# Kernel tuning notes

Hardware: AMD Instinct MI355X
Metric: run time of the kernel (lower is better)

Reference implementation:

```python
import jax, jax.numpy as jnp
import numpy as np

NUM_NOD = 6
MAX_PREV = 5
NUM_EDGE = 20  # (1+5)*5//2 + 5*(6-5)
D = 1024
H = 8
LN_EPS = 1e-6


def setup_inputs() -> dict:
    key = jax.random.key(0)
    ks = jax.random.split(key, 12)
    B, S = 8, 1024
    scale = 1.0 / np.sqrt(D)
    return {
        "inputs": jax.random.normal(ks[0], (B, S, D), jnp.float32),
        "ew": jax.random.uniform(ks[1], (NUM_NOD, 3), jnp.float32),
        "act_w": jax.random.uniform(ks[2], (NUM_NOD,), jnp.float32),
        "We": jax.random.normal(ks[3], (NUM_EDGE, D, D), jnp.float32) * scale,
        "be": jnp.zeros((NUM_EDGE, D), jnp.float32),
        "Wq": jax.random.normal(ks[4], (NUM_NOD, D, D), jnp.float32) * scale,
        "Wk": jax.random.normal(ks[5], (NUM_NOD, D, D), jnp.float32) * scale,
        "Wv": jax.random.normal(ks[6], (NUM_NOD, D, D), jnp.float32) * scale,
        "Wo": jax.random.normal(ks[7], (NUM_NOD, D, D), jnp.float32) * scale,
        "ln_g": jnp.ones((D,), jnp.float32),
        "ln_b": jnp.zeros((D,), jnp.float32),
    }


def _layernorm(x, g, b):
    mu = jnp.mean(x, axis=-1, keepdims=True)
    var = jnp.mean(jnp.square(x - mu), axis=-1, keepdims=True)
    return (x - mu) * jax.lax.rsqrt(var + LN_EPS) * g + b


def _mha(q, k, v, wq, wk, wv, wo):
    B, S, d = q.shape
    dh = d // H
    qh = (q @ wq).reshape(B, S, H, dh)
    kh = (k @ wk).reshape(B, S, H, dh)
    vh = (v @ wv).reshape(B, S, H, dh)
    scores = jnp.einsum("bqhd,bkhd->bhqk", qh, kh) / jnp.sqrt(jnp.asarray(dh, q.dtype))
    attn = jax.nn.softmax(scores, axis=-1)
    ctx = jnp.einsum("bhqk,bkhd->bqhd", attn, vh).reshape(B, S, d)
    return ctx @ wo


def reference(inputs, ew, act_w, We, be, Wq, Wk, Wv, Wo, ln_g, ln_b):
    # Fixed (deterministic) routing: node act = attention (q,k,v) for all nodes.
    # Edge op = linear (sel_ope 3). q from node c-1, k from earliest visible node,
    # v from the middle of the visible window; gated by Gumbel weights ew/act_w.
    nodes = {-1: inputs}
    lind = 0
    for c in range(NUM_NOD):
        nsrc = min(c + 1, MAX_PREV)
        snode = c - nsrc
        eq, ek, ev = lind + nsrc - 1, lind, lind + nsrc // 2
        in_q, in_k, in_v = c - 1, snode, snode + nsrc // 2
        q = ew[c, 0] * (nodes[in_q] @ We[eq] + be[eq])
        k = ew[c, 1] * (nodes[in_k] @ We[ek] + be[ek])
        v = ew[c, 2] * (nodes[in_v] @ We[ev] + be[ev])
        o = _mha(q, k, v, Wq[c], Wk[c], Wv[c], Wo[c])
        nodes[c] = act_w[c] * o + q  # gated attention + residual
        lind += nsrc
    # only node 5 is unconsumed under this routing
    out = nodes[NUM_NOD - 1]
    return _layernorm(out, ln_g, ln_b)
```

## Files before the change

### kernel.cpp

```cpp
#include <hip/hip_runtime.h>
#include <stdint.h>

#define DD 1024
#define MM 8192

typedef unsigned short u16;
typedef __attribute__((ext_vector_type(8))) short s16x8;
typedef __attribute__((ext_vector_type(4))) short s16x4;
typedef __attribute__((ext_vector_type(8))) __bf16 bf16x8;
typedef __attribute__((ext_vector_type(4))) float f32x4;

__device__ inline u16 f2bf(float f) {
  uint32_t u = __builtin_bit_cast(uint32_t, f);
  u += 0x7fffu + ((u >> 16) & 1u);
  return (u16)(u >> 16);
}
__device__ inline u16 f2bf_rn(float f) {
  return __builtin_bit_cast(u16, (__bf16)f);
}
__device__ inline float bf2f(u16 h) {
  return __builtin_bit_cast(float, (uint32_t)h << 16);
}
__device__ inline f32x4 mfma32(s16x8 a, s16x8 b, f32x4 c) {
  return __builtin_amdgcn_mfma_f32_16x16x32_bf16(
      __builtin_bit_cast(bf16x8, a), __builtin_bit_cast(bf16x8, b), c, 0, 0, 0);
}

__global__ __launch_bounds__(256) void k_cvt(const float* __restrict__ in,
                                             u16* __restrict__ out, int n8) {
  int i = blockIdx.x * 256 + threadIdx.x;
  if (i >= n8) return;
  const float4* p = (const float4*)in;
  float4 a = p[2 * i], b = p[2 * i + 1];
  union { s16x8 v; u16 u[8]; } r;
  r.u[0] = f2bf(a.x); r.u[1] = f2bf(a.y); r.u[2] = f2bf(a.z); r.u[3] = f2bf(a.w);
  r.u[4] = f2bf(b.x); r.u[5] = f2bf(b.y); r.u[6] = f2bf(b.z); r.u[7] = f2bf(b.w);
  ((s16x8*)out)[i] = r.v;
}

struct WSrcs { const float* p[7]; };
__global__ __launch_bounds__(256) void k_wtransN(WSrcs ws, u16* __restrict__ pool) {
  __shared__ u16 t[32][33];
  int m = blockIdx.z;
  const float* src = ws.p[m];
  u16* dst = pool + (size_t)m * DD * DD;
  int c0 = blockIdx.x * 32, r0 = blockIdx.y * 32;
  int tx = threadIdx.x, ty = threadIdx.y;
  #pragma unroll
  for (int j = 0; j < 4; ++j)
    t[ty + j * 8][tx] = f2bf(src[(size_t)(r0 + ty + j * 8) * DD + c0 + tx]);
  __syncthreads();
  #pragma unroll
  for (int j = 0; j < 4; ++j)
    dst[(size_t)(c0 + ty + j * 8) * DD + r0 + tx] = t[tx][ty + j * 8];
}

__global__ __launch_bounds__(256) void k_vtrans(const u16* __restrict__ vp,
                                                u16* __restrict__ vt) {
  __shared__ u16 t[32][33];
  int bh = blockIdx.z, b = bh >> 3, h = bh & 7;
  int s0 = blockIdx.x * 32, d0 = blockIdx.y * 32;
  int tx = threadIdx.x, ty = threadIdx.y;
  #pragma unroll
  for (int j = 0; j < 4; ++j)
    t[ty + j * 8][tx] = vp[(size_t)(b * 1024 + s0 + ty + j * 8) * DD + h * 128 + d0 + tx];
  __syncthreads();
  #pragma unroll
  for (int j = 0; j < 4; ++j)
    vt[((size_t)bh * 128 + d0 + ty + j * 8) * 1024 + s0 + tx] = t[tx][ty + j * 8];
}

struct GemmJob {
  const u16* A; const u16* Bt; const float* bias; const u16* resid;
  float* f32out;
  u16* out0; const float* s0p; float s0c;
  u16* out1; const float* s1p;
  u16* out2; const float* s2p;
};
struct GemmBatch { GemmJob j[3]; };

__global__ __launch_bounds__(256, 2) void k_gemmN(GemmBatch gb) {
  const GemmJob jb = gb.j[blockIdx.z];
  __shared__ u16 As[128 * 64];
  __shared__ u16 Bs[128 * 64];
  const int tid = threadIdx.x;
  const int lane = tid & 63, wave = tid >> 6;
  const int g = lane >> 4, r15 = lane & 15;
  const int m0 = blockIdx.x * 128, n0 = blockIdx.y * 128;
  const int wm = (wave >> 1) * 64, wn = (wave & 1) * 64;
  f32x4 acc[4][4] = {};
  for (int kt = 0; kt < 16; ++kt) {
    const int k0 = kt * 64;
    __syncthreads();
    #pragma unroll
    for (int i = 0; i < 4; ++i) {
      int c = tid + i * 256;
      int row = c >> 3, kc = (c & 7) ^ (row & 7);
      __builtin_amdgcn_global_load_lds(
          (__attribute__((address_space(1))) void*)(jb.A + (size_t)(m0 + row) * DD + k0 + kc * 8),
          (__attribute__((address_space(3))) void*)(As + c * 8), 16, 0, 0);
    }
    #pragma unroll
    for (int i = 0; i < 4; ++i) {
      int c = tid + i * 256;
      int row = c >> 3, kc = (c & 7) ^ (row & 7);
      __builtin_amdgcn_global_load_lds(
          (__attribute__((address_space(1))) void*)(jb.Bt + (size_t)(n0 + row) * DD + k0 + kc * 8),
          (__attribute__((address_space(3))) void*)(Bs + c * 8), 16, 0, 0);
    }
    __syncthreads();
    #pragma unroll
    for (int ks = 0; ks < 2; ++ks) {
      s16x8 af[4], bfr[4];
      #pragma unroll
      for (int f = 0; f < 4; ++f) {
        int row = wm + f * 16 + r15;
        int kc = (ks * 4 + g) ^ (row & 7);
        af[f] = *(const s16x8*)(As + row * 64 + kc * 8);
        int rowb = wn + f * 16 + r15;
        int kcb = (ks * 4 + g) ^ (rowb & 7);
        bfr[f] = *(const s16x8*)(Bs + rowb * 64 + kcb * 8);
      }
      #pragma unroll
      for (int fm = 0; fm < 4; ++fm)
        #pragma unroll
        for (int fn = 0; fn < 4; ++fn)
          acc[fm][fn] = mfma32(af[fm], bfr[fn], acc[fm][fn]);
    }
  }
  const float s0 = jb.s0c * (jb.s0p ? jb.s0p[0] : 1.0f);
  const float s1 = (jb.s1p ? jb.s1p[0] : 1.0f);
  const float s2 = (jb.s2p ? jb.s2p[0] : 1.0f);
  #pragma unroll
  for (int fm = 0; fm < 4; ++fm) {
    #pragma unroll
    for (int fn = 0; fn < 4; ++fn) {
      int col = n0 + wn + fn * 16 + r15;
      float bcol = jb.bias ? jb.bias[col] : 0.0f;
      #pragma unroll
      for (int j = 0; j < 4; ++j) {
        int row = m0 + wm + fm * 16 + g * 4 + j;
        size_t idx = (size_t)row * DD + col;
        float v = acc[fm][fn][j] + bcol;
        float v0 = s0 * v + (jb.resid ? bf2f(jb.resid[idx]) : 0.0f);
        if (jb.out0) jb.out0[idx] = f2bf(v0);
        if (jb.f32out) jb.f32out[idx] = v0;
        if (jb.out1) jb.out1[idx] = f2bf(s1 * v);
        if (jb.out2) jb.out2[idx] = f2bf(s2 * v);
      }
    }
  }
}

__global__ __launch_bounds__(256, 2) void k_attn(
    const u16* __restrict__ qp, const u16* __restrict__ kp,
    const u16* __restrict__ vt, u16* __restrict__ ctx) {
  __shared__ u16 Ks[2][64 * 128];
  __shared__ u16 Vs[2][128 * 72];
  const int lin = blockIdx.y * gridDim.x + blockIdx.x;
  const int m = lin >> 3;
  const int bh = (lin & 7) * 8 + (m & 7);
  const int q0 = (m >> 3) * 128;
  const int b = bh >> 3, h = bh & 7;
  const int tid = threadIdx.x, lane = tid & 63, wave = tid >> 6;
  const int g = lane >> 4, r15 = lane & 15;
  s16x8 qf[2][4];
  #pragma unroll
  for (int qg = 0; qg < 2; ++qg) {
    const u16* qb = qp + (size_t)(b * 1024 + q0 + wave * 32 + qg * 16 + r15) * DD + h * 128;
    #pragma unroll
    for (int kk = 0; kk < 4; ++kk) qf[qg][kk] = *(const s16x8*)(qb + kk * 32 + g * 8);
  }
  f32x4 o0[8] = {}, o1[8] = {};
  float mrow0 = -1e30f, lrow0 = 0.0f, mrow1 = -1e30f, lrow1 = 0.0f;
  const u16* kpb = kp + (size_t)b * 1024 * DD + h * 128;
  const u16* vtb = vt + (size_t)bh * 128 * 1024;

  s16x8 vreg[4];
  auto stageK = [&](int t, int buf) {
    #pragma unroll
    for (int i = 0; i < 4; ++i) {
      int c = tid + i * 256;
      int row = c >> 4, kc = (c & 15) ^ (row & 7);
      __builtin_amdgcn_global_load_lds(
          (__attribute__((address_space(1))) void*)(kpb + (size_t)(t * 64 + row) * DD + kc * 8),
          (__attribute__((address_space(3))) void*)(Ks[buf] + c * 8), 16, 0, 0);
    }
  };
  auto loadV = [&](int t) {
    #pragma unroll
    for (int i = 0; i < 4; ++i) {
      int c = tid + i * 256;
      int row = c >> 3, kc = c & 7;
      vreg[i] = *(const s16x8*)(vtb + (size_t)row * 1024 + t * 64 + kc * 8);
    }
  };
  auto writeV = [&](int buf) {
    #pragma unroll
    for (int i = 0; i < 4; ++i) {
      int c = tid + i * 256;
      int row = c >> 3, kc = c & 7;
      *(s16x8*)(Vs[buf] + row * 72 + kc * 8) = vreg[i];
    }
  };

  stageK(0, 0);
  loadV(0);
  writeV(0);
  __syncthreads();

  union pk_t { s16x8 v; u16 u[8]; };
  for (int t = 0; t < 16; ++t) {
    const int cur = t & 1;
    if (t < 15) {
      stageK(t + 1, cur ^ 1);
      loadV(t + 1);
    }
    f32x4 s0[4] = {}, s1[4] = {};
    __builtin_amdgcn_s_setprio(1);
    #pragma unroll
    for (int sub = 0; sub < 4; ++sub) {
      const int krow = sub * 16 + r15;
      #pragma unroll
      for (int kk = 0; kk < 4; ++kk) {
        int slot = (kk * 4 + g) ^ (krow & 7);
        s16x8 kf = *(const s16x8*)(Ks[cur] + krow * 128 + slot * 8);
        s0[sub] = mfma32(kf, qf[0][kk], s0[sub]);
        s1[sub] = mfma32(kf, qf[1][kk], s1[sub]);
      }
    }
    __builtin_amdgcn_s_setprio(0);
    pk_t pa0[2], pa1[2];
    {
      float tm = -1e30f;
      #pragma unroll
      for (int sub = 0; sub < 4; ++sub)
        tm = fmaxf(fmaxf(fmaxf(s0[sub][0], s0[sub][1]), fmaxf(s0[sub][2], s0[sub][3])), tm);
      tm = fmaxf(tm, __shfl_xor(tm, 16));
      tm = fmaxf(tm, __shfl_xor(tm, 32));
      if (!__all(tm - mrow0 <= 8.0f)) {
        float mnew = fmaxf(mrow0, tm);
        float corr = exp2f(mrow0 - mnew);
        lrow0 *= corr;
        #pragma unroll
        for (int j = 0; j < 4; ++j) {
          float cj = __shfl(corr, (lane & 48) + g * 4 + j);
          #pragma unroll
          for (int dt = 0; dt < 8; ++dt) o0[dt][j] *= cj;
        }
        mrow0 = mnew;
      }
      float ps = 0.0f;
      #pragma unroll
      for (int sub = 0; sub < 4; ++sub)
        #pragma unroll
        for (int j = 0; j < 4; ++j) {
          float pe = exp2f(s0[sub][j] - mrow0);
          ps += pe;
          pa0[sub >> 1].u[(sub & 1) * 4 + j] = f2bf_rn(pe);
        }
      ps += __shfl_xor(ps, 16);
      ps += __shfl_xor(ps, 32);
      lrow0 += ps;
    }
    {
      float tm = -1e30f;
      #pragma unroll
      for (int sub = 0; sub < 4; ++sub)
        tm = fmaxf(fmaxf(fmaxf(s1[sub][0], s1[sub][1]), fmaxf(s1[sub][2], s1[sub][3])), tm);
      tm = fmaxf(tm, __shfl_xor(tm, 16));
      tm = fmaxf(tm, __shfl_xor(tm, 32));
      if (!__all(tm - mrow1 <= 8.0f)) {
        float mnew = fmaxf(mrow1, tm);
        float corr = exp2f(mrow1 - mnew);
        lrow1 *= corr;
        #pragma unroll
        for (int j = 0; j < 4; ++j) {
          float cj = __shfl(corr, (lane & 48) + g * 4 + j);
          #pragma unroll
          for (int dt = 0; dt < 8; ++dt) o1[dt][j] *= cj;
        }
        mrow1 = mnew;
      }
      float ps = 0.0f;
      #pragma unroll
      for (int sub = 0; sub < 4; ++sub)
        #pragma unroll
        for (int j = 0; j < 4; ++j) {
          float pe = exp2f(s1[sub][j] - mrow1);
          ps += pe;
          pa1[sub >> 1].u[(sub & 1) * 4 + j] = f2bf_rn(pe);
        }
      ps += __shfl_xor(ps, 16);
      ps += __shfl_xor(ps, 32);
      lrow1 += ps;
    }
    if (t < 15) writeV(cur ^ 1);
    __builtin_amdgcn_s_setprio(1);
    #pragma unroll
    for (int p01 = 0; p01 < 2; ++p01) {
      #pragma unroll
      for (int dt = 0; dt < 8; ++dt) {
        union { s16x8 v; s16x4 h[2]; } vv;
        const u16* vbase = Vs[cur] + (dt * 16 + r15) * 72 + p01 * 32 + g * 4;
        vv.h[0] = *(const s16x4*)(vbase);
        vv.h[1] = *(const s16x4*)(vbase + 16);
        o0[dt] = mfma32(pa0[p01].v, vv.v, o0[dt]);
        o1[dt] = mfma32(pa1[p01].v, vv.v, o1[dt]);
      }
    }
    __builtin_amdgcn_s_setprio(0);
    __syncthreads();
  }
  {
    float inv = 1.0f / lrow0;
    #pragma unroll
    for (int j = 0; j < 4; ++j) {
      float cj = __shfl(inv, (lane & 48) + g * 4 + j);
      size_t row = (size_t)(b * 1024 + q0 + wave * 32 + g * 4 + j);
      #pragma unroll
      for (int dt = 0; dt < 8; ++dt)
        ctx[row * DD + h * 128 + dt * 16 + r15] = f2bf(o0[dt][j] * cj);
    }
  }
  {
    float inv = 1.0f / lrow1;
    #pragma unroll
    for (int j = 0; j < 4; ++j) {
      float cj = __shfl(inv, (lane & 48) + g * 4 + j);
      size_t row = (size_t)(b * 1024 + q0 + wave * 32 + 16 + g * 4 + j);
      #pragma unroll
      for (int dt = 0; dt < 8; ++dt)
        ctx[row * DD + h * 128 + dt * 16 + r15] = f2bf(o1[dt][j] * cj);
    }
  }
}

__global__ __launch_bounds__(256) void k_ln(const float* __restrict__ x,
                                            const float* __restrict__ gam,
                                            const float* __restrict__ bet,
                                            float* __restrict__ out) {
  __shared__ float red[8];
  const int row = blockIdx.x, tid = threadIdx.x, lane = tid & 63, wave = tid >> 6;
  const float4 v = ((const float4*)(x + (size_t)row * DD))[tid];
  float s = v.x + v.y + v.z + v.w;
  #pragma unroll
  for (int m = 1; m < 64; m <<= 1) s += __shfl_xor(s, m);
  if (lane == 0) red[wave] = s;
  __syncthreads();
  float mu = (red[0] + red[1] + red[2] + red[3]) * (1.0f / DD);
  float dx = v.x - mu, dy = v.y - mu, dz = v.z - mu, dw = v.w - mu;
  float q = dx * dx + dy * dy + dz * dz + dw * dw;
  #pragma unroll
  for (int m = 1; m < 64; m <<= 1) q += __shfl_xor(q, m);
  if (lane == 0) red[wave + 4] = q;
  __syncthreads();
  float var = (red[4] + red[5] + red[6] + red[7]) * (1.0f / DD);
  float inv = rsqrtf(var + 1e-6f);
  const float4 gv = ((const float4*)gam)[tid];
  const float4 bv = ((const float4*)bet)[tid];
  float4 r;
  r.x = dx * inv * gv.x + bv.x;
  r.y = dy * inv * gv.y + bv.y;
  r.z = dz * inv * gv.z + bv.z;
  r.w = dw * inv * gv.w + bv.w;
  ((float4*)(out + (size_t)row * DD))[tid] = r;
}

extern "C" void kernel_launch(void* const* d_in, const int* in_sizes, int n_in,
                              void* d_out, int out_size, void* d_ws, size_t ws_size,
                              hipStream_t stream) {
  const float* inputs = (const float*)d_in[0];
  const float* ew     = (const float*)d_in[1];
  const float* act_w  = (const float*)d_in[2];
  const float* We     = (const float*)d_in[3];
  const float* be     = (const float*)d_in[4];
  const float* Wq     = (const float*)d_in[5];
  const float* Wk     = (const float*)d_in[6];
  const float* Wv     = (const float*)d_in[7];
  const float* Wo     = (const float*)d_in[8];
  const float* ln_g   = (const float*)d_in[9];
  const float* ln_b   = (const float*)d_in[10];
  float* out = (float*)d_out;

  uint8_t* w = (uint8_t*)d_ws;
  size_t off = 0;
  auto alloc = [&](size_t bytes) {
    uint8_t* p = w + off;
    off += (bytes + 255) & ~(size_t)255;
    return p;
  };
  const size_t XB = (size_t)MM * DD * 2;
  const size_t WB = (size_t)DD * DD * 2;
  u16* Xb[6];
  for (int i = 0; i < 6; ++i) Xb[i] = (u16*)alloc(XB);
  u16* Wpool = (u16*)alloc(7 * WB);
  u16* S = (u16*)alloc(6 * XB);
  u16* S0 = S,            * S1 = S + XB / 2,     * S2 = S + XB;
  u16* S3 = S + 3 * XB / 2, * S4 = S + 2 * XB,   * S5 = S + 5 * XB / 2;
  u16* qb = S0, * kb = S1, * vb = S2, * qpb = S3, * kpb = S4, * vpb = S5;
  u16* vtb = S1, * ctxb = S2;
  float* n5 = (float*)S3;
  if (off > ws_size) {
    hipMemsetAsync(d_out, 0x7F, (size_t)out_size * 4, stream);
    return;
  }

  k_cvt<<<dim3(MM * DD / 8 / 256), 256, 0, stream>>>(inputs, Xb[0], MM * DD / 8);

  struct EG { int c, src, e, mask; };
  static const EG egs[] = {
      {0, -1, 0, 7},
      {1, 0, 2, 5},  {1, -1, 1, 2},
      {2, 1, 5, 1},  {2, -1, 3, 2},  {2, 0, 4, 4},
      {3, 2, 9, 1},  {3, -1, 6, 2},  {3, 1, 8, 4},
      {4, 3, 14, 1}, {4, -1, 10, 2}, {4, 1, 12, 4},
      {5, 4, 19, 1}, {5, 0, 15, 2},  {5, 2, 17, 4},
  };
  const float QS = 1.4426950408889634f * 0.088388347648318433f;

  for (int c = 0; c < 6; ++c) {
    WSrcs wsrc;
    int nz = 0, eslot[3], ne = 0;
    for (const auto& eg : egs)
      if (eg.c == c) { eslot[ne++] = nz; wsrc.p[nz++] = We + (size_t)eg.e * DD * DD; }
    const int sq = nz; wsrc.p[nz++] = Wq + (size_t)c * DD * DD;
    const int sk = nz; wsrc.p[nz++] = Wk + (size_t)c * DD * DD;
    const int sv = nz; wsrc.p[nz++] = Wv + (size_t)c * DD * DD;
    const int so = nz; wsrc.p[nz++] = Wo + (size_t)c * DD * DD;
    k_wtransN<<<dim3(32, 32, nz), dim3(32, 8), 0, stream>>>(wsrc, Wpool);

    GemmBatch eb{};
    int ei = 0;
    for (const auto& eg : egs) {
      if (eg.c != c) continue;
      eb.j[ei] = GemmJob{
          (eg.src < 0) ? Xb[0] : Xb[eg.src + 1],
          Wpool + (size_t)eslot[ei] * DD * DD,
          be + (size_t)eg.e * DD, nullptr, nullptr,
          (eg.mask & 1) ? qb : nullptr, ew + 3 * c + 0, 1.0f,
          (eg.mask & 2) ? kb : nullptr, ew + 3 * c + 1,
          (eg.mask & 4) ? vb : nullptr, ew + 3 * c + 2};
      ++ei;
    }
    k_gemmN<<<dim3(64, 8, ei), 256, 0, stream>>>(eb);

    GemmBatch pb{};
    pb.j[0] = GemmJob{qb, Wpool + (size_t)sq * DD * DD, nullptr, nullptr, nullptr,
                      qpb, nullptr, QS, nullptr, nullptr, nullptr, nullptr};
    pb.j[1] = GemmJob{kb, Wpool + (size_t)sk * DD * DD, nullptr, nullptr, nullptr,
                      kpb, nullptr, 1.0f, nullptr, nullptr, nullptr, nullptr};
    pb.j[2] = GemmJob{vb, Wpool + (size_t)sv * DD * DD, nullptr, nullptr, nullptr,
                      vpb, nullptr, 1.0f, nullptr, nullptr, nullptr, nullptr};
    k_gemmN<<<dim3(64, 8, 3), 256, 0, stream>>>(pb);

    k_vtrans<<<dim3(32, 4, 64), dim3(32, 8), 0, stream>>>(vpb, vtb);
    k_attn<<<dim3(8, 64), 256, 0, stream>>>(qpb, kpb, vtb, ctxb);

    GemmBatch ob{};
    ob.j[0] = GemmJob{ctxb, Wpool + (size_t)so * DD * DD, nullptr, qb,
                      (c == 5) ? n5 : nullptr,
                      (c < 5) ? Xb[c + 1] : nullptr, act_w + c, 1.0f,
                      nullptr, nullptr, nullptr, nullptr};
    k_gemmN<<<dim3(64, 8, 1), 256, 0, stream>>>(ob);
  }
  k_ln<<<dim3(MM), 256, 0, stream>>>(n5, ln_g, ln_b, out);
}
```

Before: 1.384 ms.

## Fold edge weights into K/V projection weights to skip intermediate GEMMs

For nodes 1-5, the K and V paths previously ran an edge linear (X@We) and then a projection (@Wk/Wv), which is two big 8192x1024x1024 GEMMs each. The change precomputes the combined weights We@Wk and We@Wv with small 1024^3 GEMMs, plus fused biases be@Wk and be@Wv, and applies them to the source nodes in one pass. This replaces four large GEMMs per node with two, at the cost of extra small weight GEMMs, a bias kernel and a weight conversion. The ew scale is applied in the epilogue, and the output buffer is reused as scratch for the biases. Rounding the composed weights to bf16 changes precision slightly.

```diff
diff --git a/kernel.cpp b/kernel.cpp
--- a/kernel.cpp
+++ b/kernel.cpp
@@ -38,6 +38,21 @@
   ((s16x8*)out)[i] = r.v;
 }
 
+__global__ __launch_bounds__(256) void k_cvtW(const float* __restrict__ a,
+                                              const float* __restrict__ b,
+                                              u16* __restrict__ da,
+                                              u16* __restrict__ db) {
+  int i = blockIdx.x * 256 + threadIdx.x;
+  const float* src = blockIdx.y ? b : a;
+  u16* dst = blockIdx.y ? db : da;
+  const float4* p = (const float4*)src;
+  float4 x = p[2 * i], y = p[2 * i + 1];
+  union { s16x8 v; u16 u[8]; } r;
+  r.u[0] = f2bf(x.x); r.u[1] = f2bf(x.y); r.u[2] = f2bf(x.z); r.u[3] = f2bf(x.w);
+  r.u[4] = f2bf(y.x); r.u[5] = f2bf(y.y); r.u[6] = f2bf(y.z); r.u[7] = f2bf(y.w);
+  ((s16x8*)dst)[i] = r.v;
+}
+
 struct WSrcs { const float* p[7]; };
 __global__ __launch_bounds__(256) void k_wtransN(WSrcs ws, u16* __restrict__ pool) {
   __shared__ u16 t[32][33];
@@ -53,6 +68,30 @@
   #pragma unroll
   for (int j = 0; j < 4; ++j)
     dst[(size_t)(c0 + ty + j * 8) * DD + r0 + tx] = t[tx][ty + j * 8];
+}
+
+__global__ __launch_bounds__(256) void k_bias2(const u16* __restrict__ WkT,
+                                               const float* __restrict__ bek,
+                                               const u16* __restrict__ WvT,
+                                               const float* __restrict__ bev,
+                                               float* __restrict__ bk,
+                                               float* __restrict__ bv) {
+  const u16* W = blockIdx.y ? WvT : WkT;
+  const float* be = blockIdx.y ? bev : bek;
+  float* out = blockIdx.y ? bv : bk;
+  int n = blockIdx.x * 256 + threadIdx.x;
+  const u16* row = W + (size_t)n * DD;
+  float acc = 0.0f;
+  for (int k8 = 0; k8 < DD / 8; ++k8) {
+    s16x8 w = *(const s16x8*)(row + k8 * 8);
+    const float4* bp = (const float4*)(be + k8 * 8);
+    float4 b0 = bp[0], b1 = bp[1];
+    acc += b0.x * bf2f((u16)w[0]) + b0.y * bf2f((u16)w[1]) +
+           b0.z * bf2f((u16)w[2]) + b0.w * bf2f((u16)w[3]) +
+           b1.x * bf2f((u16)w[4]) + b1.y * bf2f((u16)w[5]) +
+           b1.z * bf2f((u16)w[6]) + b1.w * bf2f((u16)w[7]);
+  }
+  out[n] = acc;
 }
 
 __global__ __launch_bounds__(256) void k_vtrans(const u16* __restrict__ vp,
@@ -401,6 +440,8 @@
   u16* qb = S0, * kb = S1, * vb = S2, * qpb = S3, * kpb = S4, * vpb = S5;
   u16* vtb = S1, * ctxb = S2;
   float* n5 = (float*)S3;
+  u16* WeK = S1, * WeV = S1 + DD * DD;
+  float* bkv = out;
   if (off > ws_size) {
     hipMemsetAsync(d_out, 0x7F, (size_t)out_size * 4, stream);
     return;
@@ -408,57 +449,74 @@
 
   k_cvt<<<dim3(MM * DD / 8 / 256), 256, 0, stream>>>(inputs, Xb[0], MM * DD / 8);
 
-  struct EG { int c, src, e, mask; };
-  static const EG egs[] = {
-      {0, -1, 0, 7},
-      {1, 0, 2, 5},  {1, -1, 1, 2},
-      {2, 1, 5, 1},  {2, -1, 3, 2},  {2, 0, 4, 4},
-      {3, 2, 9, 1},  {3, -1, 6, 2},  {3, 1, 8, 4},
-      {4, 3, 14, 1}, {4, -1, 10, 2}, {4, 1, 12, 4},
-      {5, 4, 19, 1}, {5, 0, 15, 2},  {5, 2, 17, 4},
+  struct Node { int sq, eq, sk, ek, sv, ev; };
+  static const Node route[6] = {
+      {-1, 0, -1, 0, -1, 0},
+      {0, 2, -1, 1, 0, 2},
+      {1, 5, -1, 3, 0, 4},
+      {2, 9, -1, 6, 1, 8},
+      {3, 14, -1, 10, 1, 12},
+      {4, 19, -1, 15, 2, 17},
   };
   const float QS = 1.4426950408889634f * 0.088388347648318433f;
+  auto src = [&](int s) { return (s < 0) ? Xb[0] : Xb[s + 1]; };
+  u16* slot[7];
+  for (int i = 0; i < 7; ++i) slot[i] = Wpool + (size_t)i * DD * DD;
 
   for (int c = 0; c < 6; ++c) {
-    WSrcs wsrc;
-    int nz = 0, eslot[3], ne = 0;
-    for (const auto& eg : egs)
-      if (eg.c == c) { eslot[ne++] = nz; wsrc.p[nz++] = We + (size_t)eg.e * DD * DD; }
-    const int sq = nz; wsrc.p[nz++] = Wq + (size_t)c * DD * DD;
-    const int sk = nz; wsrc.p[nz++] = Wk + (size_t)c * DD * DD;
-    const int sv = nz; wsrc.p[nz++] = Wv + (size_t)c * DD * DD;
-    const int so = nz; wsrc.p[nz++] = Wo + (size_t)c * DD * DD;
-    k_wtransN<<<dim3(32, 32, nz), dim3(32, 8), 0, stream>>>(wsrc, Wpool);
-
-    GemmBatch eb{};
-    int ei = 0;
-    for (const auto& eg : egs) {
-      if (eg.c != c) continue;
-      eb.j[ei] = GemmJob{
-          (eg.src < 0) ? Xb[0] : Xb[eg.src + 1],
-          Wpool + (size_t)eslot[ei] * DD * DD,
-          be + (size_t)eg.e * DD, nullptr, nullptr,
-          (eg.mask & 1) ? qb : nullptr, ew + 3 * c + 0, 1.0f,
-          (eg.mask & 2) ? kb : nullptr, ew + 3 * c + 1,
-          (eg.mask & 4) ? vb : nullptr, ew + 3 * c + 2};
-      ++ei;
-    }
-    k_gemmN<<<dim3(64, 8, ei), 256, 0, stream>>>(eb);
-
-    GemmBatch pb{};
-    pb.j[0] = GemmJob{qb, Wpool + (size_t)sq * DD * DD, nullptr, nullptr, nullptr,
-                      qpb, nullptr, QS, nullptr, nullptr, nullptr, nullptr};
-    pb.j[1] = GemmJob{kb, Wpool + (size_t)sk * DD * DD, nullptr, nullptr, nullptr,
-                      kpb, nullptr, 1.0f, nullptr, nullptr, nullptr, nullptr};
-    pb.j[2] = GemmJob{vb, Wpool + (size_t)sv * DD * DD, nullptr, nullptr, nullptr,
-                      vpb, nullptr, 1.0f, nullptr, nullptr, nullptr, nullptr};
-    k_gemmN<<<dim3(64, 8, 3), 256, 0, stream>>>(pb);
+    const Node& nd = route[c];
+    WSrcs ws5;
+    ws5.p[0] = We + (size_t)nd.eq * DD * DD;
+    ws5.p[1] = Wq + (size_t)c * DD * DD;
+    ws5.p[2] = Wk + (size_t)c * DD * DD;
+    ws5.p[3] = Wv + (size_t)c * DD * DD;
+    ws5.p[4] = Wo + (size_t)c * DD * DD;
+    k_wtransN<<<dim3(32, 32, 5), dim3(32, 8), 0, stream>>>(ws5, Wpool);
+
+    if (c == 0) {
+      GemmBatch eb{};
+      eb.j[0] = GemmJob{src(nd.sq), slot[0], be + (size_t)nd.eq * DD, nullptr, nullptr,
+                        qb, ew + 3 * c + 0, 1.0f, kb, ew + 3 * c + 1, vb, ew + 3 * c + 2};
+      k_gemmN<<<dim3(64, 8, 1), 256, 0, stream>>>(eb);
+      GemmBatch pb{};
+      pb.j[0] = GemmJob{qb, slot[1], nullptr, nullptr, nullptr,
+                        qpb, nullptr, QS, nullptr, nullptr, nullptr, nullptr};
+      pb.j[1] = GemmJob{kb, slot[2], nullptr, nullptr, nullptr,
+                        kpb, nullptr, 1.0f, nullptr, nullptr, nullptr, nullptr};
+      pb.j[2] = GemmJob{vb, slot[3], nullptr, nullptr, nullptr,
+                        vpb, nullptr, 1.0f, nullptr, nullptr, nullptr, nullptr};
+      k_gemmN<<<dim3(64, 8, 3), 256, 0, stream>>>(pb);
+    } else {
+      k_cvtW<<<dim3(DD * DD / 8 / 256, 2), 256, 0, stream>>>(
+          We + (size_t)nd.ek * DD * DD, We + (size_t)nd.ev * DD * DD, WeK, WeV);
+      GemmBatch cb{};
+      cb.j[0] = GemmJob{slot[2], WeK, nullptr, nullptr, nullptr,
+                        slot[5], nullptr, 1.0f, nullptr, nullptr, nullptr, nullptr};
+      cb.j[1] = GemmJob{slot[3], WeV, nullptr, nullptr, nullptr,
+                        slot[6], nullptr, 1.0f, nullptr, nullptr, nullptr, nullptr};
+      k_gemmN<<<dim3(8, 8, 2), 256, 0, stream>>>(cb);
+      k_bias2<<<dim3(4, 2), 256, 0, stream>>>(slot[2], be + (size_t)nd.ek * DD,
+                                              slot[3], be + (size_t)nd.ev * DD,
+                                              bkv, bkv + DD);
+      GemmBatch mb{};
+      mb.j[0] = GemmJob{src(nd.sq), slot[0], be + (size_t)nd.eq * DD, nullptr, nullptr,
+                        qb, ew + 3 * c + 0, 1.0f, nullptr, nullptr, nullptr, nullptr};
+      mb.j[1] = GemmJob{src(nd.sk), slot[5], bkv, nullptr, nullptr,
+                        kpb, ew + 3 * c + 1, 1.0f, nullptr, nullptr, nullptr, nullptr};
+      mb.j[2] = GemmJob{src(nd.sv), slot[6], bkv + DD, nullptr, nullptr,
+                        vpb, ew + 3 * c + 2, 1.0f, nullptr, nullptr, nullptr, nullptr};
+      k_gemmN<<<dim3(64, 8, 3), 256, 0, stream>>>(mb);
+      GemmBatch qp{};
+      qp.j[0] = GemmJob{qb, slot[1], nullptr, nullptr, nullptr,
+                        qpb, nullptr, QS, nullptr, nullptr, nullptr, nullptr};
+      k_gemmN<<<dim3(64, 8, 1), 256, 0, stream>>>(qp);
+    }
 
     k_vtrans<<<dim3(32, 4, 64), dim3(32, 8), 0, stream>>>(vpb, vtb);
     k_attn<<<dim3(8, 64), 256, 0, stream>>>(qpb, kpb, vtb, ctxb);
 
     GemmBatch ob{};
-    ob.j[0] = GemmJob{ctxb, Wpool + (size_t)so * DD * DD, nullptr, qb,
+    ob.j[0] = GemmJob{ctxb, slot[4], nullptr, qb,
                       (c == 5) ? n5 : nullptr,
                       (c < 5) ? Xb[c + 1] : nullptr, act_w + c, 1.0f,
                       nullptr, nullptr, nullptr, nullptr};
```

Measured after the change: 1.444 ms. +4.3%, slower.
